# Kernel tuning notes

Hardware: AMD Instinct MI355X
Metric: run time of the kernel (lower is better)

Reference implementation:

```python
import jax, jax.numpy as jnp
import numpy as np

DIM = 256
CTX_DIM = 256
HEADS = 32
DIM_HEAD = 32
INNER = HEADS * DIM_HEAD


def mish(x):
    return x * jnp.tanh(jax.nn.softplus(x))


def setup_inputs() -> dict:
    key = jax.random.key(0)
    ks = jax.random.split(key, 16)
    B, Lq, Lp = 16, 128, 512
    s = 0.02
    return {
        "x": jax.random.normal(ks[0], (B * Lq, DIM), jnp.float32),
        "context": jax.random.normal(ks[1], (B * Lp, CTX_DIM), jnp.float32),
        "batch_dis": jax.random.normal(ks[2], (B, Lp, Lq, 3), jnp.float32),
        "batch_dis_emb": jax.random.normal(ks[3], (B, Lp, Lq, HEADS), jnp.float32),
        "protein_len": Lp,
        "ligand_len": Lq,
        # params ([in, out] layout, torch Linear transposed)
        "W_qk": jax.random.normal(ks[4], (DIM, INNER), jnp.float32) * s,
        "W_v": jax.random.normal(ks[5], (DIM, INNER), jnp.float32) * s,
        "W_cqk": jax.random.normal(ks[6], (CTX_DIM, INNER), jnp.float32) * s,
        "W_cv": jax.random.normal(ks[7], (CTX_DIM, INNER), jnp.float32) * s,
        "W_m1": jax.random.normal(ks[8], (2 * HEADS, 4 * HEADS), jnp.float32) * s,
        "W_m2": jax.random.normal(ks[9], (4 * HEADS, 2 * HEADS), jnp.float32) * s,
        "b_m2": jnp.zeros((2 * HEADS,), jnp.float32),
        "W_o": jax.random.normal(ks[10], (INNER, DIM), jnp.float32) * s,
        "b_o": jnp.zeros((DIM,), jnp.float32),
        "W_d1": jax.random.normal(ks[11], (HEADS, 2 * HEADS), jnp.float32) * s,
        "b_d1": jnp.zeros((2 * HEADS,), jnp.float32),
        "W_d2": jax.random.normal(ks[12], (2 * HEADS, HEADS), jnp.float32) * s,
        "b_d2": jnp.zeros((HEADS,), jnp.float32),
    }


def reference(x, context, batch_dis, batch_dis_emb, protein_len, ligand_len,
              W_qk, W_v, W_cqk, W_cv, W_m1, W_m2, b_m2, W_o, b_o,
              W_d1, b_d1, W_d2, b_d2):
    h, dh = HEADS, DIM_HEAD
    scale = dh ** -0.5
    B = x.shape[0] // ligand_len
    # projections; split heads: [B, L, h, dh]
    qk = (x @ W_qk).reshape(B, ligand_len, h, dh)
    cqk = (context @ W_cqk).reshape(B, protein_len, h, dh)
    cv = (context @ W_cv).reshape(B, protein_len, h, dh)
    # ligand->protein attention scores: [B, h, Lq, Lp]
    sim = jnp.einsum('bihd,bjhd->bhij', qk, cqk) * scale
    # distance-embedding channels: [B, Lp, Lq, h] -> [B, h, Lq, Lp]
    dis = jnp.transpose(batch_dis_emb, (0, 3, 2, 1))
    s = jnp.concatenate([sim, dis], axis=1)           # [B, 2h, Lq, Lp]
    s = jnp.moveaxis(s, 1, -1)                        # [B, Lq, Lp, 2h]
    s = mish(s @ W_m1) @ W_m2 + b_m2                  # attn_mlp over channel dim
    attn = jax.nn.softmax(s, axis=2)                  # softmax over protein (j)
    # first h heads attend into context values
    out = jnp.einsum('bijh,bjhd->bihd', attn[..., :h], cv)
    out = out.reshape(B * ligand_len, h * dh) @ W_o + b_o   # [N_lig, dim]
    # last h heads aggregate 3D distance vectors
    out_dis = jnp.einsum('bijh,bjid->bidh', attn[..., h:], batch_dis)
    out_dis = out_dis.reshape(B * ligand_len, 3, h)
    out_dis = mish(out_dis @ W_d1 + b_d1) @ W_d2 + b_d2      # [N_lig, 3, h]
    return out, out_dis
```

## Files before the change

kernel.cpp:

```cpp
#include <hip/hip_runtime.h>

typedef unsigned short u16;
typedef unsigned int   u32;
typedef __attribute__((ext_vector_type(8))) short bf16x8;
typedef __attribute__((ext_vector_type(4))) float f32x4;

#define MFMA_BF16 __builtin_amdgcn_mfma_f32_16x16x32_bf16
#define LOG2E 1.4426950408889634f

__device__ __forceinline__ u16 f2bf(float f) {
    u32 x = __builtin_bit_cast(u32, f);
    u32 r = (x + 0x7fffu + ((x >> 16) & 1u)) >> 16;
    return (u16)r;
}
__device__ __forceinline__ u32 cvt_pk_bf16(float lo, float hi) {
    u32 r;
    asm("v_cvt_pk_bf16_f32 %0, %1, %2" : "=v"(r) : "v"(lo), "v"(hi));
    return r;
}
__device__ __forceinline__ float exp2_asm(float x) {
    float r;
    asm("v_exp_f32 %0, %1" : "=v"(r) : "v"(x));
    return r;
}
__device__ __forceinline__ float rcp_asm(float x) {
    float r;
    asm("v_rcp_f32 %0, %1" : "=v"(r) : "v"(x));
    return r;
}
__device__ __forceinline__ float mishf(float x) {
    float e = exp2_asm(x * LOG2E);
    float p = 1.f + e;
    float d = __builtin_fmaf(p, p, 1.f);
    float r = __builtin_fmaf(-2.f, rcp_asm(d), 1.f);
    return x * r;
}

__global__ __launch_bounds__(256) void proj_fused(
    const float* __restrict__ x,   const float* __restrict__ Wqk,  u16* __restrict__ qk_ws,
    const float* __restrict__ ctx, const float* __restrict__ Wcqk, u16* __restrict__ cqk_ws,
    const float* __restrict__ Wcv, u16* __restrict__ cvT,
    const float* __restrict__ Wo,  const float* __restrict__ W1,   const float* __restrict__ W2,
    u16* __restrict__ WoT, u16* __restrict__ w1b, u16* __restrict__ w2b,
    float scale)
{
    __shared__ __align__(16) char smem[18432];
    const int id = blockIdx.x;
    const int tid = threadIdx.x;

    if (id >= 1152) {
        const int bb = id - 1152, t = tid;
        if (bb < 256) {
#pragma unroll
            for (int kk = 0; kk < 4; ++kk)
                WoT[(size_t)t * 1024 + bb * 4 + kk] = f2bf(Wo[(size_t)(bb * 4 + kk) * 256 + t]);
        } else {
            for (int u = 0; u < 32; ++u) {
                int idx = t + 256 * u;
                int j = idx & 7, lane = (idx >> 3) & 63, f = idx >> 9;
                int n = lane & 15, q = lane >> 4, ntc = f & 7, ks = f >> 3;
                w1b[idx] = f2bf(W1[(ks * 32 + q * 8 + j) * 128 + ntc * 16 + n]);
            }
            for (int u = 0; u < 32; ++u) {
                int idx = t + 256 * u;
                int j = idx & 7, lane = (idx >> 3) & 63, f = idx >> 9;
                int n = lane & 15, q = lane >> 4, ot = f & 3, ks = f >> 2;
                int k = q * 8 + j;
                int ch = ((k & 1) << 4) | (k >> 1);
                w2b[idx] = f2bf(W2[(ks * 32 + ch) * 64 + ot * 16 + n] * LOG2E);
            }
        }
        return;
    }

    u16* As = (u16*)smem;
    u16* Bf = (u16*)(smem + 10240);

    const float* A; const float* W; u16* C = qk_ws;
    int bx, by; bool cv = false; float sc = 1.0f;
    if (id < 128)      { A = x;   W = Wqk;  C = qk_ws;  bx = id & 7; by = id >> 3; sc = scale; }
    else if (id < 640) { A = ctx; W = Wcqk; C = cqk_ws; int i2 = id - 128; bx = i2 & 7; by = i2 >> 3; }
    else               { A = ctx; W = Wcv;              int i2 = id - 640; bx = i2 & 7; by = i2 >> 3; cv = true; }

    const int K = 256, N = 1024;
    const int lane = tid & 63, wv = tid >> 6;
    const int qd = lane >> 4, ln = lane & 15;
    const int m0 = by * 128, n0 = bx * 128;

    f32x4 acc[2][8];
#pragma unroll
    for (int a = 0; a < 2; ++a)
#pragma unroll
        for (int nt = 0; nt < 8; ++nt) acc[a][nt] = (f32x4){0.f, 0.f, 0.f, 0.f};

    for (int k0 = 0; k0 < K; k0 += 32) {
        {
            int r = tid >> 1, kh = (tid & 1) * 16;
            const float* ap = A + (size_t)(m0 + r) * K + k0 + kh;
            float4 a0 = ((const float4*)ap)[0];
            float4 a1 = ((const float4*)ap)[1];
            float4 a2 = ((const float4*)ap)[2];
            float4 a3 = ((const float4*)ap)[3];
            uint4 p0, p1;
            p0.x = cvt_pk_bf16(a0.x, a0.y);
            p0.y = cvt_pk_bf16(a0.z, a0.w);
            p0.z = cvt_pk_bf16(a1.x, a1.y);
            p0.w = cvt_pk_bf16(a1.z, a1.w);
            p1.x = cvt_pk_bf16(a2.x, a2.y);
            p1.y = cvt_pk_bf16(a2.z, a2.w);
            p1.z = cvt_pk_bf16(a3.x, a3.y);
            p1.w = cvt_pk_bf16(a3.z, a3.w);
            *(uint4*)&As[r * 40 + kh]     = p0;
            *(uint4*)&As[r * 40 + kh + 8] = p1;
        }
        {
            int ntA = tid >> 6, q = (tid >> 4) & 3, nn = tid & 15;
#pragma unroll
            for (int h = 0; h < 2; ++h) {
                int nt = ntA + h * 4;
                const float* wp = W + (size_t)(k0 + q * 8) * N + n0 + nt * 16 + nn;
                float w0 = wp[0], w1 = wp[(size_t)1 * N], w2 = wp[(size_t)2 * N], w3 = wp[(size_t)3 * N];
                float w4 = wp[(size_t)4 * N], w5 = wp[(size_t)5 * N], w6 = wp[(size_t)6 * N], w7 = wp[(size_t)7 * N];
                uint4 u;
                u.x = cvt_pk_bf16(w0, w1);
                u.y = cvt_pk_bf16(w2, w3);
                u.z = cvt_pk_bf16(w4, w5);
                u.w = cvt_pk_bf16(w6, w7);
                *(uint4*)&Bf[(nt * 64 + q * 16 + nn) * 8] = u;
            }
        }
        __syncthreads();
        bf16x8 af0 = *(const bf16x8*)&As[(wv * 32 + ln) * 40 + qd * 8];
        bf16x8 af1 = *(const bf16x8*)&As[(wv * 32 + 16 + ln) * 40 + qd * 8];
#pragma unroll
        for (int nt = 0; nt < 8; ++nt) {
            bf16x8 bfr = *(const bf16x8*)&Bf[(nt * 64 + lane) * 8];
            acc[0][nt] = MFMA_BF16(af0, bfr, acc[0][nt], 0, 0, 0);
            acc[1][nt] = MFMA_BF16(af1, bfr, acc[1][nt], 0, 0, 0);
        }
        __syncthreads();
    }

    if (!cv) {
#pragma unroll
        for (int a = 0; a < 2; ++a)
#pragma unroll
            for (int nt = 0; nt < 8; ++nt) {
                u32 pk0 = cvt_pk_bf16(acc[a][nt][0] * sc, acc[a][nt][1] * sc);
                u32 pk1 = cvt_pk_bf16(acc[a][nt][2] * sc, acc[a][nt][3] * sc);
                size_t base = (size_t)(m0 + wv * 32 + a * 16 + qd * 4) * N + n0 + nt * 16 + ln;
                C[base]               = (u16)pk0;
                C[base + (size_t)N]   = (u16)(pk0 >> 16);
                C[base + (size_t)2*N] = (u16)pk1;
                C[base + (size_t)3*N] = (u16)(pk1 >> 16);
            }
    } else {
        const int b = m0 >> 9, jt = m0 & 511;
        u16* T = (u16*)smem;
#pragma unroll
        for (int h = 0; h < 2; ++h) {
            if (h) __syncthreads();
#pragma unroll
            for (int a = 0; a < 2; ++a)
#pragma unroll
                for (int t2 = 0; t2 < 4; ++t2) {
                    int nt = h * 4 + t2;
                    int chl = t2 * 16 + ln;
                    int row = wv * 32 + a * 16 + qd * 4;
                    uint2 pk;
                    pk.x = cvt_pk_bf16(acc[a][nt][0], acc[a][nt][1]);
                    pk.y = cvt_pk_bf16(acc[a][nt][2], acc[a][nt][3]);
                    *(uint2*)&T[chl * 136 + row] = pk;
                }
            __syncthreads();
            {
                int chl = tid >> 2, jseg = (tid & 3) * 32;
                const uint4* src = (const uint4*)&T[chl * 136 + jseg];
                u16* dst = cvT + ((size_t)(b * 1024 + n0 + h * 64 + chl)) * 512 + jt + jseg;
                ((uint4*)dst)[0] = src[0];
                ((uint4*)dst)[1] = src[1];
                ((uint4*)dst)[2] = src[2];
                ((uint4*)dst)[3] = src[3];
            }
        }
    }
}

__global__ __launch_bounds__(256, 1) void attn5(
    const u16* __restrict__ qk,
    const u16* __restrict__ cqk,
    const u16* __restrict__ cvT,
    const float* __restrict__ bde,
    const float* __restrict__ bdis,
    const u16* __restrict__ w1b, const u16* __restrict__ w2b,
    const float* __restrict__ b2,
    float* __restrict__ partial)
{
    __shared__ __align__(16) char smem[76288];
    u16*   ES  = (u16*)smem;
    u16*   MT  = (u16*)(smem + 20480);
    float* BD  = (float*)(smem + 30720);
    u16*   EST = (u16*)(smem + 34816);
    u16*   W1B = (u16*)(smem + 59904);

    const int tid = threadIdx.x;
    const int lane = tid & 63, wv = tid >> 6;
    const int qd = lane >> 4, ln = lane & 15;
    const int nblk = blockIdx.x;
    const int xcd = nblk & 7, g = nblk >> 3;
    const int b = xcd * 2 + (g & 1);
    const int r2 = g >> 1;
    const int it = r2 >> 2, jq = r2 & 3;
    const int i0 = it * 16;
    const int pidx = (b * 8 + it) * 4 + jq;

    for (int k = tid; k < 4096; k += 256) ((u32*)W1B)[k] = ((const u32*)w1b)[k];

    float b2r[4];
#pragma unroll
    for (int ot = 0; ot < 4; ++ot) b2r[ot] = b2[ot * 16 + ln] * LOG2E;

    bf16x8 qkf[8];
#pragma unroll
    for (int hh = 0; hh < 8; ++hh) {
        int h = wv * 8 + hh;
        qkf[hh] = *(const bf16x8*)(qk + ((size_t)(b * 128 + i0 + ln)) * 1024 + h * 32 + qd * 8);
    }

    const int ii = tid & 15, jj = tid >> 4;

    bf16x8 cqk_pf[8];
    float4 bde_pf[8];
    float bdp0, bdp1, bdp2;
    {
        const u16* crow = cqk + (size_t)(b * 512 + jq * 128 + ln) * 1024 + qd * 8;
#pragma unroll
        for (int hh = 0; hh < 8; ++hh)
            cqk_pf[hh] = *(const bf16x8*)(crow + (wv * 8 + hh) * 32);
#pragma unroll
        for (int s2 = 0; s2 < 4; ++s2) {
            const float* dps = bde + (((size_t)(b * 512 + jq * 128 + ln)) * 128 + i0 + wv * 4 + s2) * 32 + qd * 8;
            bde_pf[s2 * 2]     = ((const float4*)dps)[0];
            bde_pf[s2 * 2 + 1] = ((const float4*)dps)[1];
        }
        const float* sp = bdis + ((size_t)(b * 512 + jq * 128 + jj) * 128 + i0 + ii) * 3;
        bdp0 = sp[0]; bdp1 = sp[1]; bdp2 = sp[2];
        float* dp2 = &BD[(ii * 16 + jj) * 4];
        dp2[0] = bdp0; dp2[1] = bdp1; dp2[2] = bdp2;
    }

    f32x4 oacc[8][2];
#pragma unroll
    for (int a = 0; a < 8; ++a)
#pragma unroll
        for (int c = 0; c < 2; ++c) oacc[a][c] = (f32x4){0.f, 0.f, 0.f, 0.f};
    float dn[4][4] = {};
    float dd[4][3][2] = {};

    __syncthreads();

#pragma clang loop unroll(disable)
    for (int ps = 0; ps < 8; ++ps) {
        const int jg0 = jq * 128 + ps * 16;

        {
            bf16x8 cqk_use[8];
#pragma unroll
            for (int hh = 0; hh < 8; ++hh) cqk_use[hh] = cqk_pf[hh];
#pragma unroll
            for (int hh = 0; hh < 4; ++hh) {
                const int h0 = wv * 8 + hh * 2;
                f32x4 c0 = (f32x4){0.f, 0.f, 0.f, 0.f}, c1 = c0;
                c0 = MFMA_BF16(qkf[hh * 2],     cqk_use[hh * 2],     c0, 0, 0, 0);
                c1 = MFMA_BF16(qkf[hh * 2 + 1], cqk_use[hh * 2 + 1], c1, 0, 0, 0);
#pragma unroll
                for (int r = 0; r < 4; ++r)
                    *(u32*)&ES[((qd * 4 + r) * 16 + ln) * 40 + h0] = cvt_pk_bf16(c0[r], c1[r]);
            }
        }
        __syncthreads();

        const int psn = (ps < 7) ? ps + 1 : 7;
        const int jgn = jq * 128 + psn * 16;
        float4 bde_use[8];
#pragma unroll
        for (int k = 0; k < 8; ++k) bde_use[k] = bde_pf[k];
        {
            const u16* crow = cqk + (size_t)(b * 512 + jgn + ln) * 1024 + qd * 8;
#pragma unroll
            for (int hh = 0; hh < 8; ++hh)
                cqk_pf[hh] = *(const bf16x8*)(crow + (wv * 8 + hh) * 32);
#pragma unroll
            for (int s2 = 0; s2 < 4; ++s2) {
                const float* dps = bde + (((size_t)(b * 512 + jgn + ln)) * 128 + i0 + wv * 4 + s2) * 32 + qd * 8;
                bde_pf[s2 * 2]     = ((const float4*)dps)[0];
                bde_pf[s2 * 2 + 1] = ((const float4*)dps)[1];
            }
            const float* sp = bdis + ((size_t)(b * 512 + jgn + jj) * 128 + i0 + ii) * 3;
            bdp0 = sp[0]; bdp1 = sp[1]; bdp2 = sp[2];
        }

#pragma unroll
        for (int s = 0; s < 4; ++s) {
            const int i_loc = wv * 4 + s;
            bf16x8 af0 = *(const bf16x8*)&ES[(i_loc * 16 + ln) * 40 + qd * 8];
            bf16x8 af1;
            {
                float4 a0 = bde_use[s * 2];
                float4 a1 = bde_use[s * 2 + 1];
                uint4 u;
                u.x = cvt_pk_bf16(a0.x, a0.y);
                u.y = cvt_pk_bf16(a0.z, a0.w);
                u.z = cvt_pk_bf16(a1.x, a1.y);
                u.w = cvt_pk_bf16(a1.z, a1.w);
                af1 = __builtin_bit_cast(bf16x8, u);
            }
            f32x4 uacc[4];
#pragma unroll
            for (int ot = 0; ot < 4; ++ot) uacc[ot] = (f32x4){0.f, 0.f, 0.f, 0.f};
#pragma unroll
            for (int cg = 0; cg < 4; ++cg) {
                u16* mtp = MT + wv * 1280 + (cg & 1) * 640;
                bf16x8 w00 = *(const bf16x8*)&W1B[((cg * 2 + 0) * 64 + lane) * 8];
                bf16x8 w01 = *(const bf16x8*)&W1B[((cg * 2 + 1) * 64 + lane) * 8];
                bf16x8 w10 = *(const bf16x8*)&W1B[((8 + cg * 2 + 0) * 64 + lane) * 8];
                bf16x8 w11 = *(const bf16x8*)&W1B[((8 + cg * 2 + 1) * 64 + lane) * 8];
                f32x4 t0 = (f32x4){0.f, 0.f, 0.f, 0.f}, t1 = t0;
                t0 = MFMA_BF16(af0, w00, t0, 0, 0, 0);
                t0 = MFMA_BF16(af1, w10, t0, 0, 0, 0);
                t1 = MFMA_BF16(af0, w01, t1, 0, 0, 0);
                t1 = MFMA_BF16(af1, w11, t1, 0, 0, 0);
#pragma unroll
                for (int r = 0; r < 4; ++r) {
                    u32 pk = cvt_pk_bf16(mishf(t0[r]), mishf(t1[r]));
                    *(u32*)&mtp[(qd * 4 + r) * 40 + (ln << 1)] = pk;
                }
                bf16x8 ta = *(const bf16x8*)&mtp[ln * 40 + qd * 8];
#pragma unroll
                for (int ot = 0; ot < 4; ++ot) {
                    bf16x8 wf = *(const bf16x8*)(w2b + ((size_t)(cg * 4 + ot) * 64 + lane) * 8);
                    uacc[ot] = MFMA_BF16(ta, wf, uacc[ot], 0, 0, 0);
                }
            }
            float Ev[4][4];
#pragma unroll
            for (int ot = 0; ot < 4; ++ot) {
#pragma unroll
                for (int r = 0; r < 4; ++r) Ev[ot][r] = exp2_asm(uacc[ot][r] + b2r[ot]);
                dn[s][ot] += (Ev[ot][0] + Ev[ot][1]) + (Ev[ot][2] + Ev[ot][3]);
            }
#pragma unroll
            for (int r = 0; r < 4; ++r) {
                float4 bp = *(const float4*)&BD[(i_loc * 16 + qd * 4 + r) * 4];
                dd[s][0][0] += Ev[2][r] * bp.x; dd[s][0][1] += Ev[3][r] * bp.x;
                dd[s][1][0] += Ev[2][r] * bp.y; dd[s][1][1] += Ev[3][r] * bp.y;
                dd[s][2][0] += Ev[2][r] * bp.z; dd[s][2][1] += Ev[3][r] * bp.z;
            }
#pragma unroll
            for (int ot = 0; ot < 2; ++ot) {
                const int base = (ot * 16 + ln) * 392 + i_loc * 24 + qd * 4;
                *(u32*)&EST[base]     = cvt_pk_bf16(Ev[ot][0], Ev[ot][1]);
                *(u32*)&EST[base + 2] = cvt_pk_bf16(Ev[ot][2], Ev[ot][3]);
            }
        }
        __syncthreads();

        {
            float* dp2 = &BD[(ii * 16 + jj) * 4];
            dp2[0] = bdp0; dp2[1] = bdp1; dp2[2] = bdp2;
        }
#pragma unroll
        for (int hh = 0; hh < 8; ++hh) {
            const int h = wv * 8 + hh;
            bf16x8 af = (bf16x8){0, 0, 0, 0, 0, 0, 0, 0};
            if (qd < 2) af = *(const bf16x8*)&EST[h * 392 + ln * 24 + qd * 8];
#pragma unroll
            for (int nt = 0; nt < 2; ++nt) {
                bf16x8 bfr = (bf16x8){0, 0, 0, 0, 0, 0, 0, 0};
                if (qd < 2)
                    bfr = *(const bf16x8*)(cvT + ((size_t)(b * 1024 + h * 32 + nt * 16 + ln)) * 512 + jg0 + qd * 8);
                oacc[hh][nt] = MFMA_BF16(af, bfr, oacc[hh][nt], 0, 0, 0);
            }
        }
    }

    float* P = partial + (size_t)pidx * 18944;
#pragma unroll
    for (int hh = 0; hh < 8; ++hh)
#pragma unroll
        for (int nt = 0; nt < 2; ++nt)
#pragma unroll
            for (int r = 0; r < 4; ++r)
                P[(size_t)(qd * 4 + r) * 1024 + (wv * 8 + hh) * 32 + nt * 16 + ln] = oacc[hh][nt][r];
#pragma unroll
    for (int s = 0; s < 4; ++s)
#pragma unroll
        for (int ot = 0; ot < 4; ++ot) {
            float v = dn[s][ot];
            v += __shfl_xor(v, 16, 64);
            v += __shfl_xor(v, 32, 64);
            if (qd == 0) P[16384 + (wv * 4 + s) * 64 + ot * 16 + ln] = v;
        }
#pragma unroll
    for (int s = 0; s < 4; ++s)
#pragma unroll
        for (int d = 0; d < 3; ++d)
#pragma unroll
            for (int o = 0; o < 2; ++o) {
                float v = dd[s][d][o];
                v += __shfl_xor(v, 16, 64);
                v += __shfl_xor(v, 32, 64);
                if (qd == 0) P[17408 + (wv * 4 + s) * 96 + d * 32 + o * 16 + ln] = v;
            }
}

__global__ __launch_bounds__(256, 2) void finalize(
    const float* __restrict__ partial, const u16* __restrict__ WoT,
    const float* __restrict__ bo,
    const float* __restrict__ Wd1, const float* __restrict__ bd1,
    const float* __restrict__ Wd2, const float* __restrict__ bd2,
    float* __restrict__ out0, float* __restrict__ out1)
{
    __shared__ float denomL[1024];
    __shared__ u16 preL[16 * 1032];
    __shared__ float odisL[1536];
    __shared__ float r1L[3072];

    const int tid = threadIdx.x;
    const int f = blockIdx.x;
    const int b = f >> 3, it = f & 7;
    const int row0 = b * 128 + it * 16;
    const float* P0 = partial + (size_t)(f * 4 + 0) * 18944;
    const float* P1 = partial + (size_t)(f * 4 + 1) * 18944;
    const float* P2 = partial + (size_t)(f * 4 + 2) * 18944;
    const float* P3 = partial + (size_t)(f * 4 + 3) * 18944;

    for (int k = tid; k < 1024; k += 256)
        denomL[k] = P0[16384 + k] + P1[16384 + k] + P2[16384 + k] + P3[16384 + k];
    __syncthreads();

    {
        const int h = tid >> 3;
#pragma unroll
        for (int i = 0; i < 16; ++i) {
            float4 a = *(const float4*)&P0[(size_t)i * 1024 + tid * 4];
            float4 bq = *(const float4*)&P1[(size_t)i * 1024 + tid * 4];
            float4 c = *(const float4*)&P2[(size_t)i * 1024 + tid * 4];
            float4 d = *(const float4*)&P3[(size_t)i * 1024 + tid * 4];
            float rdn = 1.f / denomL[i * 64 + h];
            u32 p0 = cvt_pk_bf16((a.x + bq.x + c.x + d.x) * rdn, (a.y + bq.y + c.y + d.y) * rdn);
            u32 p1 = cvt_pk_bf16((a.z + bq.z + c.z + d.z) * rdn, (a.w + bq.w + c.w + d.w) * rdn);
            *(uint2*)(void*)&preL[i * 1032 + tid * 4] = make_uint2(p0, p1);
        }
    }
    for (int idx = tid; idx < 1536; idx += 256) {
        int i = idx / 96, rm = idx % 96, h = rm & 31;
        odisL[idx] = (P0[17408 + idx] + P1[17408 + idx] + P2[17408 + idx] + P3[17408 + idx])
                     / denomL[i * 64 + 32 + h];
    }
    __syncthreads();

    {
        const int lane = tid & 63, wv = tid >> 6;
        const int qd = lane >> 4, ln = lane & 15;
        f32x4 acc[4];
#pragma unroll
        for (int nt = 0; nt < 4; ++nt) acc[nt] = (f32x4){0.f, 0.f, 0.f, 0.f};
#pragma clang loop unroll(disable)
        for (int ks = 0; ks < 32; ++ks) {
            bf16x8 af = *(const bf16x8*)&preL[ln * 1032 + ks * 32 + qd * 8];
#pragma unroll
            for (int nt = 0; nt < 4; ++nt) {
                bf16x8 wf = *(const bf16x8*)(WoT + ((size_t)(wv * 64 + nt * 16 + ln)) * 1024 + ks * 32 + qd * 8);
                acc[nt] = MFMA_BF16(af, wf, acc[nt], 0, 0, 0);
            }
        }
#pragma unroll
        for (int nt = 0; nt < 4; ++nt) {
            int col = wv * 64 + nt * 16 + ln;
            float bv = bo[col];
#pragma unroll
            for (int r = 0; r < 4; ++r)
                out0[(size_t)(row0 + qd * 4 + r) * 256 + col] = acc[nt][r] + bv;
        }
    }

    for (int idx = tid; idx < 3072; idx += 256) {
        int i = idx / 192, rm = idx % 192, d = rm / 64, c = rm & 63;
        float t = bd1[c];
#pragma unroll
        for (int hh = 0; hh < 32; ++hh)
            t += odisL[i * 96 + d * 32 + hh] * Wd1[hh * 64 + c];
        r1L[idx] = mishf(t);
    }
    __syncthreads();
    for (int idx = tid; idx < 1536; idx += 256) {
        int i = idx / 96, rm = idx % 96, d = rm >> 5, h = rm & 31;
        float v = bd2[h];
#pragma unroll
        for (int c = 0; c < 64; ++c)
            v += r1L[i * 192 + d * 64 + c] * Wd2[c * 32 + h];
        out1[(size_t)(row0 + i) * 96 + d * 32 + h] = v;
    }
}

extern "C" void kernel_launch(void* const* d_in, const int* in_sizes, int n_in,
                              void* d_out, int out_size, void* d_ws, size_t ws_size,
                              hipStream_t stream) {
    const float* x    = (const float*)d_in[0];
    const float* ctx  = (const float*)d_in[1];
    const float* bdis = (const float*)d_in[2];
    const float* bde  = (const float*)d_in[3];
    const float* Wqk  = (const float*)d_in[6];
    const float* Wcqk = (const float*)d_in[8];
    const float* Wcv  = (const float*)d_in[9];
    const float* Wm1  = (const float*)d_in[10];
    const float* Wm2  = (const float*)d_in[11];
    const float* bm2  = (const float*)d_in[12];
    const float* Wo   = (const float*)d_in[13];
    const float* bo   = (const float*)d_in[14];
    const float* Wd1  = (const float*)d_in[15];
    const float* bd1  = (const float*)d_in[16];
    const float* Wd2  = (const float*)d_in[17];
    const float* bd2  = (const float*)d_in[18];

    char* ws = (char*)d_ws;
    u16* qk_ws  = (u16*)(ws);
    u16* cqk_ws = (u16*)(ws + 4194304);
    u16* cvT_ws = (u16*)(ws + 20971520);
    u16* w1b    = (u16*)(ws + 37748736);
    u16* w2b    = (u16*)(ws + 37765120);
    u16* WoT    = (u16*)(ws + 37781504);
    float* part = (float*)(ws + 38305792);

    float* out0 = (float*)d_out;
    float* out1 = out0 + (size_t)2048 * 256;

    const float SCALE = 0.17677669529663687f;

    proj_fused<<<1409, 256, 0, stream>>>(x, Wqk, qk_ws, ctx, Wcqk, cqk_ws,
                                         Wcv, cvT_ws, Wo, Wm1, Wm2,
                                         WoT, w1b, w2b, SCALE);
    attn5<<<512, 256, 0, stream>>>(qk_ws, cqk_ws, cvT_ws, bde, bdis, w1b, w2b, bm2, part);
    finalize<<<128, 256, 0, stream>>>(part, WoT, bo, Wd1, bd1, Wd2, bd2, out0, out1);
}
```

Baseline: 506.4 us.

## Halve protein-axis split in attention kernel and prefetch context values early

The attention kernel now splits the protein dimension into two halves instead of four, so each block runs 16 protein sub-steps and the grid shrinks from 512 to 256 blocks. The finalize kernel correspondingly sums two partials instead of four, which cuts partial-buffer writes and reads. The context-value fragments for the output MFMA are also loaded into registers earlier in each iteration, so their latency overlaps the MLP and softmax work. In exchange, 256 blocks may underfill the GPU's compute units, and the extra prefetch registers may increase register pressure.

```diff
diff --git a/kernel.cpp b/kernel.cpp
--- a/kernel.cpp
+++ b/kernel.cpp
@@ -210,9 +210,10 @@
     const int xcd = nblk & 7, g = nblk >> 3;
     const int b = xcd * 2 + (g & 1);
     const int r2 = g >> 1;
-    const int it = r2 >> 2, jq = r2 & 3;
+    const int it = r2 >> 1, jh = r2 & 1;
     const int i0 = it * 16;
-    const int pidx = (b * 8 + it) * 4 + jq;
+    const int jbase = jh * 256;
+    const int pidx = (b * 8 + it) * 2 + jh;
 
     for (int k = tid; k < 4096; k += 256) ((u32*)W1B)[k] = ((const u32*)w1b)[k];
 
@@ -233,17 +234,17 @@
     float4 bde_pf[8];
     float bdp0, bdp1, bdp2;
     {
-        const u16* crow = cqk + (size_t)(b * 512 + jq * 128 + ln) * 1024 + qd * 8;
+        const u16* crow = cqk + (size_t)(b * 512 + jbase + ln) * 1024 + qd * 8;
 #pragma unroll
         for (int hh = 0; hh < 8; ++hh)
             cqk_pf[hh] = *(const bf16x8*)(crow + (wv * 8 + hh) * 32);
 #pragma unroll
         for (int s2 = 0; s2 < 4; ++s2) {
-            const float* dps = bde + (((size_t)(b * 512 + jq * 128 + ln)) * 128 + i0 + wv * 4 + s2) * 32 + qd * 8;
+            const float* dps = bde + (((size_t)(b * 512 + jbase + ln)) * 128 + i0 + wv * 4 + s2) * 32 + qd * 8;
             bde_pf[s2 * 2]     = ((const float4*)dps)[0];
             bde_pf[s2 * 2 + 1] = ((const float4*)dps)[1];
         }
-        const float* sp = bdis + ((size_t)(b * 512 + jq * 128 + jj) * 128 + i0 + ii) * 3;
+        const float* sp = bdis + ((size_t)(b * 512 + jbase + jj) * 128 + i0 + ii) * 3;
         bdp0 = sp[0]; bdp1 = sp[1]; bdp2 = sp[2];
         float* dp2 = &BD[(ii * 16 + jj) * 4];
         dp2[0] = bdp0; dp2[1] = bdp1; dp2[2] = bdp2;
@@ -260,8 +261,8 @@
     __syncthreads();
 
 #pragma clang loop unroll(disable)
-    for (int ps = 0; ps < 8; ++ps) {
-        const int jg0 = jq * 128 + ps * 16;
+    for (int ps = 0; ps < 16; ++ps) {
+        const int jg0 = jbase + ps * 16;
 
         {
             bf16x8 cqk_use[8];
@@ -280,11 +281,12 @@
         }
         __syncthreads();
 
-        const int psn = (ps < 7) ? ps + 1 : 7;
-        const int jgn = jq * 128 + psn * 16;
+        const int psn = (ps < 15) ? ps + 1 : 15;
+        const int jgn = jbase + psn * 16;
         float4 bde_use[8];
 #pragma unroll
         for (int k = 0; k < 8; ++k) bde_use[k] = bde_pf[k];
+        bf16x8 cvt_pf[16];
         {
             const u16* crow = cqk + (size_t)(b * 512 + jgn + ln) * 1024 + qd * 8;
 #pragma unroll
@@ -298,6 +300,17 @@
             }
             const float* sp = bdis + ((size_t)(b * 512 + jgn + jj) * 128 + i0 + ii) * 3;
             bdp0 = sp[0]; bdp1 = sp[1]; bdp2 = sp[2];
+#pragma unroll
+            for (int hh = 0; hh < 8; ++hh) {
+                const int h = wv * 8 + hh;
+#pragma unroll
+                for (int nt = 0; nt < 2; ++nt) {
+                    cvt_pf[hh * 2 + nt] = (bf16x8){0, 0, 0, 0, 0, 0, 0, 0};
+                    if (qd < 2)
+                        cvt_pf[hh * 2 + nt] = *(const bf16x8*)(cvT +
+                            ((size_t)(b * 1024 + h * 32 + nt * 16 + ln)) * 512 + jg0 + qd * 8);
+                }
+            }
         }
 
 #pragma unroll
@@ -375,12 +388,8 @@
             bf16x8 af = (bf16x8){0, 0, 0, 0, 0, 0, 0, 0};
             if (qd < 2) af = *(const bf16x8*)&EST[h * 392 + ln * 24 + qd * 8];
 #pragma unroll
-            for (int nt = 0; nt < 2; ++nt) {
-                bf16x8 bfr = (bf16x8){0, 0, 0, 0, 0, 0, 0, 0};
-                if (qd < 2)
-                    bfr = *(const bf16x8*)(cvT + ((size_t)(b * 1024 + h * 32 + nt * 16 + ln)) * 512 + jg0 + qd * 8);
-                oacc[hh][nt] = MFMA_BF16(af, bfr, oacc[hh][nt], 0, 0, 0);
-            }
+            for (int nt = 0; nt < 2; ++nt)
+                oacc[hh][nt] = MFMA_BF16(af, cvt_pf[hh * 2 + nt], oacc[hh][nt], 0, 0, 0);
         }
     }
 
@@ -430,13 +439,11 @@
     const int f = blockIdx.x;
     const int b = f >> 3, it = f & 7;
     const int row0 = b * 128 + it * 16;
-    const float* P0 = partial + (size_t)(f * 4 + 0) * 18944;
-    const float* P1 = partial + (size_t)(f * 4 + 1) * 18944;
-    const float* P2 = partial + (size_t)(f * 4 + 2) * 18944;
-    const float* P3 = partial + (size_t)(f * 4 + 3) * 18944;
+    const float* P0 = partial + (size_t)(f * 2 + 0) * 18944;
+    const float* P1 = partial + (size_t)(f * 2 + 1) * 18944;
 
     for (int k = tid; k < 1024; k += 256)
-        denomL[k] = P0[16384 + k] + P1[16384 + k] + P2[16384 + k] + P3[16384 + k];
+        denomL[k] = P0[16384 + k] + P1[16384 + k];
     __syncthreads();
 
     {
@@ -445,17 +452,15 @@
         for (int i = 0; i < 16; ++i) {
             float4 a = *(const float4*)&P0[(size_t)i * 1024 + tid * 4];
             float4 bq = *(const float4*)&P1[(size_t)i * 1024 + tid * 4];
-            float4 c = *(const float4*)&P2[(size_t)i * 1024 + tid * 4];
-            float4 d = *(const float4*)&P3[(size_t)i * 1024 + tid * 4];
             float rdn = 1.f / denomL[i * 64 + h];
-            u32 p0 = cvt_pk_bf16((a.x + bq.x + c.x + d.x) * rdn, (a.y + bq.y + c.y + d.y) * rdn);
-            u32 p1 = cvt_pk_bf16((a.z + bq.z + c.z + d.z) * rdn, (a.w + bq.w + c.w + d.w) * rdn);
+            u32 p0 = cvt_pk_bf16((a.x + bq.x) * rdn, (a.y + bq.y) * rdn);
+            u32 p1 = cvt_pk_bf16((a.z + bq.z) * rdn, (a.w + bq.w) * rdn);
             *(uint2*)(void*)&preL[i * 1032 + tid * 4] = make_uint2(p0, p1);
         }
     }
     for (int idx = tid; idx < 1536; idx += 256) {
         int i = idx / 96, rm = idx % 96, h = rm & 31;
-        odisL[idx] = (P0[17408 + idx] + P1[17408 + idx] + P2[17408 + idx] + P3[17408 + idx])
+        odisL[idx] = (P0[17408 + idx] + P1[17408 + idx])
                      / denomL[i * 64 + 32 + h];
     }
     __syncthreads();
@@ -541,6 +546,6 @@
     proj_fused<<<1409, 256, 0, stream>>>(x, Wqk, qk_ws, ctx, Wcqk, cqk_ws,
                                          Wcv, cvT_ws, Wo, Wm1, Wm2,
                                          WoT, w1b, w2b, SCALE);
-    attn5<<<512, 256, 0, stream>>>(qk_ws, cqk_ws, cvT_ws, bde, bdis, w1b, w2b, bm2, part);
+    attn5<<<256, 256, 0, stream>>>(qk_ws, cqk_ws, cvT_ws, bde, bdis, w1b, w2b, bm2, part);
     finalize<<<128, 256, 0, stream>>>(part, WoT, bo, Wd1, bd1, Wd2, bd2, out0, out1);
 }
```

Measured after the change: 473.1 us. 6.6% less time.
